# Kernel optimization log

Measured on AMD Instinct MI355X. Metric: run time of the kernel, lower is better.

The kernel has to match this reference:

```python
import jax, jax.numpy as jnp
import numpy as np

N, D, T, H, R = 1024, 6, 60, 64, 64
NEG = -10000.0
SLOPE = 0.01  # default LeakyReLU negative slope


def setup_inputs() -> dict:
    key = jax.random.key(0)
    ks = jax.random.split(key, 12)
    x = jax.random.normal(ks[0], (N, D * T), jnp.float32)
    relation_matrix = (jax.random.uniform(ks[1], (N, N, R)) < 0.02).astype(jnp.float32)
    s = 1.0 / np.sqrt(H)
    inp = {
        "x": x,
        "relation_matrix": relation_matrix,
        "W": jax.random.normal(ks[2], (2 * H + R, 1), jnp.float32) / np.sqrt(2 * H + R),
        "b": jnp.zeros((), jnp.float32),
        "fc_w": jax.random.normal(ks[3], (1, 2 * H), jnp.float32) * s,
        "fc_b": jnp.zeros((1,), jnp.float32),
        "Wih0": jax.random.normal(ks[4], (3 * H, D), jnp.float32) * s,
        "Whh0": jax.random.normal(ks[5], (3 * H, H), jnp.float32) * s,
        "bih0": jax.random.normal(ks[6], (3 * H,), jnp.float32) * s,
        "bhh0": jax.random.normal(ks[7], (3 * H,), jnp.float32) * s,
        "Wih1": jax.random.normal(ks[8], (3 * H, H), jnp.float32) * s,
        "Whh1": jax.random.normal(ks[9], (3 * H, H), jnp.float32) * s,
        "bih1": jax.random.normal(ks[10], (3 * H,), jnp.float32) * s,
        "bhh1": jax.random.normal(ks[11], (3 * H,), jnp.float32) * s,
    }
    return inp


def gru_layer(x, Wih, Whh, bih, bhh):
    # x: [N, T, in] -> outputs [N, T, H]; torch GRU gate order: r, z, n
    xg = x @ Wih.T + bih            # [N, T, 3H], input gates precomputed
    xg = jnp.swapaxes(xg, 0, 1)     # [T, N, 3H]

    def step(h, g):
        hg = h @ Whh.T + bhh
        xr, xz, xn = jnp.split(g, 3, axis=-1)
        hr, hz, hn = jnp.split(hg, 3, axis=-1)
        r = jax.nn.sigmoid(xr + hr)
        z = jax.nn.sigmoid(xz + hz)
        n = jnp.tanh(xn + r * hn)
        h = (1.0 - z) * n + z * h
        return h, h

    h0 = jnp.zeros((x.shape[0], Whh.shape[1]), x.dtype)
    _, ys = jax.lax.scan(step, h0, xg)
    return jnp.swapaxes(ys, 0, 1)   # [N, T, H]


def reference(x, relation_matrix, W, b, fc_w, fc_b,
              Wih0, Whh0, bih0, bhh0, Wih1, Whh1, bih1, bhh1):
    # [N, D*T] -> [N, T, D]
    xs = jnp.transpose(x.reshape(x.shape[0], D, -1), (0, 2, 1))
    h = gru_layer(xs, Wih0, Whh0, bih0, bhh0)
    h = gru_layer(h, Wih1, Whh1, bih1, bhh1)
    h = h[:, -1, :]                 # [N, H] last-step hidden

    # score[i,j] = cat(h_i, h_j, rel_ij) @ W + b, computed without the NxNx(2H+R) concat
    Wv = W[:, 0]
    sa = h @ Wv[:H]                              # [N]  (ei part)
    sb = h @ Wv[H:2 * H]                         # [N]  (hidden_batch part)
    sr = jnp.einsum('ijr,r->ij', relation_matrix, Wv[2 * H:])  # [N, N]
    weight = sa[:, None] + sb[None, :] + sr + b
    weight = jnp.where(weight >= 0, weight, SLOPE * weight)    # LeakyReLU

    mask = (relation_matrix.sum(-1) != 0).astype(h.dtype)      # [N, N]
    temp = mask * weight
    temp = jnp.where(temp == 0, NEG, temp)                     # faithful to torch ==0 fill
    valid = jax.nn.softmax(temp, axis=1) * mask

    agg = valid @ h                                            # [N, H]
    hidden = jnp.concatenate([h, agg], axis=1)                 # [N, 2H]
    pred_all = (hidden @ fc_w.T + fc_b).squeeze()
    return pred_all
```

## Files before the change

kernel.cpp:

```cpp
#include <hip/hip_runtime.h>
#include <cstddef>

#define NN 1024
#define DD 6
#define TT 60
#define HH 64
#define NEGV  (-10000.0f)
#define SLOPEV (0.01f)
#define GRUB 64
#define RELB 448
#define RELW (RELB * 8)
#define NGRP (NN * NN / 64)

#define BH0O  0
#define BH1O  1152
#define XH    2304
#define HEP   6144
#define SMEMF 7232

typedef _Float16 v8h __attribute__((ext_vector_type(8)));
typedef float    v4f __attribute__((ext_vector_type(4)));

#define MF(a, b, c) __builtin_amdgcn_mfma_f32_16x16x32_f16((a), (b), (c), 0, 0, 0)

__device__ __forceinline__ float sig_(float x)  { return 1.0f / (1.0f + __expf(-x)); }
__device__ __forceinline__ float tanh_(float x) { return 1.0f - 2.0f / (__expf(2.0f * x) + 1.0f); }
__device__ __forceinline__ float bcf_(const float a, const float b) {
    return __builtin_bit_cast(float, __builtin_amdgcn_cvt_pkrtz(a, b));
}
__device__ __forceinline__ v8h zero8() {
    v8h r;
    #pragma unroll
    for (int j = 0; j < 8; ++j) r[j] = (_Float16)0.f;
    return r;
}
__device__ __forceinline__ v8h pack8(const float* __restrict__ p) {
    v8h r;
    #pragma unroll
    for (int j = 0; j < 8; ++j) r[j] = (_Float16)p[j];
    return r;
}
__device__ __forceinline__ v8h pack6(const float* __restrict__ p) {
    v8h r = zero8();
    #pragma unroll
    for (int j = 0; j < 6; ++j) r[j] = (_Float16)p[j];
    return r;
}

__global__ __launch_bounds__(512)
void k_main(const float* __restrict__ x, const float* __restrict__ rel,
            const float* __restrict__ W, const float* __restrict__ fc_w,
            const float* __restrict__ Wih0, const float* __restrict__ Whh0,
            const float* __restrict__ bih0, const float* __restrict__ bhh0,
            const float* __restrict__ Wih1, const float* __restrict__ Whh1,
            const float* __restrict__ bih1, const float* __restrict__ bhh1,
            float* __restrict__ sa, float* __restrict__ sb,
            float* __restrict__ hdot, float* __restrict__ hb,
            float* __restrict__ sr, float* __restrict__ ssum)
{
    __shared__ float smem[SMEMF];
    const int tid = threadIdx.x;

    if (blockIdx.x >= GRUB) {
        const int lane = tid & 63;
        const int l16  = lane & 15;
        const int sub  = lane >> 4;
        const float4 wv4 = *(const float4*)(W + 2 * HH + l16 * 4);
        const unsigned wid = (unsigned)(blockIdx.x - GRUB) * 8 + (tid >> 6);
        for (unsigned g = wid; g < (unsigned)NGRP; g += RELW) {
            const float4* bp = (const float4*)(rel + (size_t)g * 4096) + lane;
            float4 v[16];
            #pragma unroll
            for (int q = 0; q < 16; ++q) v[q] = bp[q * 64];
            float dt[16], sm[16];
            #pragma unroll
            for (int q = 0; q < 16; ++q) {
                dt[q] = v[q].x * wv4.x + v[q].y * wv4.y + v[q].z * wv4.z + v[q].w * wv4.w;
                sm[q] = (v[q].x + v[q].y) + (v[q].z + v[q].w);
            }
            #pragma unroll
            for (int m = 1; m <= 8; m <<= 1) {
                #pragma unroll
                for (int q = 0; q < 16; ++q) {
                    dt[q] += __shfl_xor(dt[q], m);
                    sm[q] += __shfl_xor(sm[q], m);
                }
            }
            if (l16 == 0) {
                #pragma unroll
                for (int q = 0; q < 16; ++q) {
                    const unsigned p = g * 64 + q * 4 + sub;
                    sr[p]   = dt[q];
                    ssum[p] = sm[q];
                }
            }
        }
        return;
    }

    const int w    = tid >> 6;
    const int lane = tid & 63;
    const int quad = lane >> 4;
    const int mc   = lane & 15;
    const int nb   = blockIdx.x * 16;
    const bool isL0 = (w < 4);
    const int wt   = isL0 ? w : (w - 4);

    for (int idx = tid; idx < TT * 16; idx += 512) {
        const int t = idx >> 4, n = idx & 15;
        const float* xp = x + (size_t)(nb + n) * (DD * TT) + t;
        float4 pk;
        pk.x = bcf_(xp[0],   xp[60]);
        pk.y = bcf_(xp[120], xp[180]);
        pk.z = bcf_(xp[240], xp[300]);
        pk.w = 0.f;
        *(float4*)(smem + XH + idx * 4) = pk;
    }
    for (int idx = tid; idx < 2304; idx += 512) smem[idx] = 0.f;

    const int r0row = 16 * wt + mc;
    const int zrow  = 64 + 16 * wt + mc;
    const int nrow  = 128 + 16 * wt + mc;
    v8h F0 = zero8(), F1 = zero8(), F2 = zero8(), F3 = zero8();
    v8h F4 = zero8(), F5 = zero8(), F6 = zero8(), F7 = zero8();
    v8h F8 = zero8(), F9 = zero8(), F10 = zero8(), F11 = zero8();
    v8h Xr = zero8(), Xz = zero8(), Xn = zero8();
    if (isL0) {
        F0 = pack8(Whh0 + (size_t)r0row * HH + quad * 8);
        F1 = pack8(Whh0 + (size_t)r0row * HH + 32 + quad * 8);
        F2 = pack8(Whh0 + (size_t)zrow  * HH + quad * 8);
        F3 = pack8(Whh0 + (size_t)zrow  * HH + 32 + quad * 8);
        F4 = pack8(Whh0 + (size_t)nrow  * HH + quad * 8);
        F5 = pack8(Whh0 + (size_t)nrow  * HH + 32 + quad * 8);
        if (quad == 0) {
            Xr = pack6(Wih0 + r0row * DD);
            Xz = pack6(Wih0 + zrow  * DD);
            Xn = pack6(Wih0 + nrow  * DD);
        }
    } else {
        F0 = pack8(Wih1 + (size_t)r0row * HH + quad * 8);
        F1 = pack8(Wih1 + (size_t)r0row * HH + 32 + quad * 8);
        F2 = pack8(Whh1 + (size_t)r0row * HH + quad * 8);
        F3 = pack8(Whh1 + (size_t)r0row * HH + 32 + quad * 8);
        F4 = pack8(Wih1 + (size_t)zrow * HH + quad * 8);
        F5 = pack8(Wih1 + (size_t)zrow * HH + 32 + quad * 8);
        F6 = pack8(Whh1 + (size_t)zrow * HH + quad * 8);
        F7 = pack8(Whh1 + (size_t)zrow * HH + 32 + quad * 8);
        F8 = pack8(Wih1 + (size_t)nrow * HH + quad * 8);
        F9 = pack8(Wih1 + (size_t)nrow * HH + 32 + quad * 8);
        F10 = pack8(Whh1 + (size_t)nrow * HH + quad * 8);
        F11 = pack8(Whh1 + (size_t)nrow * HH + 32 + quad * 8);
    }

    float bR[4], bZ[4], bXn[4], bHn[4];
    #pragma unroll
    for (int e = 0; e < 4; ++e) {
        const int cr = 16 * wt + quad * 4 + e;
        if (isL0) {
            bR[e]  = bih0[cr] + bhh0[cr];
            bZ[e]  = bih0[64 + cr] + bhh0[64 + cr];
            bXn[e] = bih0[128 + cr];
            bHn[e] = bhh0[128 + cr];
        } else {
            bR[e]  = bih1[cr] + bhh1[cr];
            bZ[e]  = bih1[64 + cr] + bhh1[64 + cr];
            bXn[e] = bih1[128 + cr];
            bHn[e] = bhh1[128 + cr];
        }
    }

    float hp[4] = {0.f, 0.f, 0.f, 0.f};
    __syncthreads();

    auto ldb = [&](const float* basep, int win) -> v8h {
        return __builtin_bit_cast(v8h,
            *(const float4*)(basep + mc * 36 + win * 16 + quad * 4));
    };
    auto sth = [&](float* basep) {
        float2 pk;
        pk.x = bcf_(hp[0], hp[1]);
        pk.y = bcf_(hp[2], hp[3]);
        *(float2*)(basep + mc * 36 + 8 * wt + 2 * quad) = pk;
    };
    auto gupd = [&](const v4f& cr, const v4f& cz, const v4f& cx, const v4f& ch) {
        #pragma unroll
        for (int e = 0; e < 4; ++e) {
            const float r  = sig_(cr[e]);
            const float z  = sig_(cz[e]);
            const float nv = tanh_(cx[e] + r * ch[e]);
            hp[e] = (1.f - z) * nv + z * hp[e];
        }
    };

    for (int i = 0; i <= TT; ++i) {
        const int rbo = (i & 1) * 576;
        const int wbo = 576 - rbo;
        if (isL0) {
            if (i < TT) {
                const v8h b0 = ldb(smem + BH0O + rbo, 0);
                const v8h b1 = ldb(smem + BH0O + rbo, 1);
                const float4 xl = *(const float4*)(smem + XH + (i * 16 + mc) * 4);
                v8h bx = zero8();
                if (quad == 0) bx = __builtin_bit_cast(v8h, xl);

                v4f cr = {bR[0], bR[1], bR[2], bR[3]};
                cr = MF(F0, b0, cr); cr = MF(F1, b1, cr); cr = MF(Xr, bx, cr);
                v4f cz = {bZ[0], bZ[1], bZ[2], bZ[3]};
                cz = MF(F2, b0, cz); cz = MF(F3, b1, cz); cz = MF(Xz, bx, cz);
                v4f ch = {bHn[0], bHn[1], bHn[2], bHn[3]};
                ch = MF(F4, b0, ch); ch = MF(F5, b1, ch);
                v4f cx = {bXn[0], bXn[1], bXn[2], bXn[3]};
                cx = MF(Xn, bx, cx);

                gupd(cr, cz, cx, ch);
                sth(smem + BH0O + wbo);
            }
        } else {
            if (i >= 1) {
                const v8h g0 = ldb(smem + BH0O + rbo, 0);
                const v8h g1 = ldb(smem + BH0O + rbo, 1);
                const v8h g2 = ldb(smem + BH1O + rbo, 0);
                const v8h g3 = ldb(smem + BH1O + rbo, 1);

                v4f cr = {bR[0], bR[1], bR[2], bR[3]};
                cr = MF(F0, g0, cr); cr = MF(F1, g1, cr);
                cr = MF(F2, g2, cr); cr = MF(F3, g3, cr);
                v4f cz = {bZ[0], bZ[1], bZ[2], bZ[3]};
                cz = MF(F4, g0, cz); cz = MF(F5, g1, cz);
                cz = MF(F6, g2, cz); cz = MF(F7, g3, cz);
                v4f cx = {bXn[0], bXn[1], bXn[2], bXn[3]};
                cx = MF(F8, g0, cx); cx = MF(F9, g1, cx);
                v4f ch = {bHn[0], bHn[1], bHn[2], bHn[3]};
                ch = MF(F10, g2, ch); ch = MF(F11, g3, ch);

                gupd(cr, cz, cx, ch);
                sth(smem + BH1O + wbo);
            }
        }
        __syncthreads();
    }

    if (!isL0) {
        #pragma unroll
        for (int e = 0; e < 4; ++e)
            smem[HEP + (16 * wt + quad * 4 + e) * 17 + mc] = hp[e];
    }
    __syncthreads();
    if (isL0) {
        const int n = lane >> 2, p = lane & 3;
        const float* __restrict__ wp = (w == 0) ? W : (w == 1) ? (W + HH)
                                     : (w == 2) ? fc_w : (fc_w + HH);
        float v = 0.f;
        #pragma unroll
        for (int q = 0; q < 16; ++q) {
            const int j = p * 16 + q;
            v += smem[HEP + j * 17 + n] * wp[j];
        }
        v += __shfl_down(v, 2);
        v += __shfl_down(v, 1);
        if (p == 0) {
            float* dst = (w == 0) ? sa : (w == 1) ? sb : (w == 2) ? hdot : hb;
            dst[nb + n] = v;
        }
    }
}

__global__ __launch_bounds__(256)
void k2(const float* __restrict__ sa, const float* __restrict__ sb,
        const float* __restrict__ hdot, const float* __restrict__ hb,
        const float* __restrict__ sr, const float* __restrict__ ssum,
        const float* __restrict__ bscal, const float* __restrict__ fc_b,
        float* __restrict__ out)
{
    __shared__ float red[12];
    const int i   = blockIdx.x;
    const int tid = threadIdx.x;
    const int j4  = tid * 4;
    const float sai = sa[i] + bscal[0];

    const float4 srv = *(const float4*)(sr   + (size_t)i * NN + j4);
    const float4 ssv = *(const float4*)(ssum + (size_t)i * NN + j4);
    const float4 sbv = *(const float4*)(sb + j4);

    float tv[4], mk[4];
    float mloc = -3.4e38f;
    {
        const float srq[4] = {srv.x, srv.y, srv.z, srv.w};
        const float ssq[4] = {ssv.x, ssv.y, ssv.z, ssv.w};
        const float sbq[4] = {sbv.x, sbv.y, sbv.z, sbv.w};
        #pragma unroll
        for (int q = 0; q < 4; ++q) {
            float wv = sai + sbq[q] + srq[q];
            wv = (wv >= 0.0f) ? wv : SLOPEV * wv;
            const float m = (ssq[q] != 0.0f) ? 1.0f : 0.0f;
            float tt = m * wv;
            tt = (tt == 0.0f) ? NEGV : tt;
            tv[q] = tt; mk[q] = m;
            mloc = fmaxf(mloc, tt);
        }
    }
    #pragma unroll
    for (int off = 32; off >= 1; off >>= 1) mloc = fmaxf(mloc, __shfl_xor(mloc, off));
    if ((tid & 63) == 0) red[tid >> 6] = mloc;
    __syncthreads();
    const float mx = fmaxf(fmaxf(red[0], red[1]), fmaxf(red[2], red[3]));

    const float4 hbv = *(const float4*)(hb + j4);
    const float hbq[4] = {hbv.x, hbv.y, hbv.z, hbv.w};
    float sloc = 0.0f, vloc = 0.0f;
    #pragma unroll
    for (int q = 0; q < 4; ++q) {
        const float e = __expf(tv[q] - mx);
        sloc += e;
        vloc += e * mk[q] * hbq[q];
    }
    #pragma unroll
    for (int off = 32; off >= 1; off >>= 1) {
        sloc += __shfl_xor(sloc, off);
        vloc += __shfl_xor(vloc, off);
    }
    if ((tid & 63) == 0) { red[4 + (tid >> 6)] = sloc; red[8 + (tid >> 6)] = vloc; }
    __syncthreads();
    if (tid == 0) {
        const float denom = red[4] + red[5] + red[6] + red[7];
        const float vsum  = red[8] + red[9] + red[10] + red[11];
        out[i] = hdot[i] + vsum / denom + fc_b[0];
    }
}

extern "C" void kernel_launch(void* const* d_in, const int* in_sizes, int n_in,
                              void* d_out, int out_size, void* d_ws, size_t ws_size,
                              hipStream_t stream)
{
    const float* x     = (const float*)d_in[0];
    const float* rel   = (const float*)d_in[1];
    const float* W     = (const float*)d_in[2];
    const float* b     = (const float*)d_in[3];
    const float* fc_w  = (const float*)d_in[4];
    const float* fc_b  = (const float*)d_in[5];
    const float* Wih0  = (const float*)d_in[6];
    const float* Whh0  = (const float*)d_in[7];
    const float* bih0  = (const float*)d_in[8];
    const float* bhh0  = (const float*)d_in[9];
    const float* Wih1  = (const float*)d_in[10];
    const float* Whh1  = (const float*)d_in[11];
    const float* bih1  = (const float*)d_in[12];
    const float* bhh1  = (const float*)d_in[13];

    float* ws   = (float*)d_ws;
    float* sa   = ws;
    float* sb   = sa   + NN;
    float* hdot = sb   + NN;
    float* hb   = hdot + NN;
    float* sr   = hb   + NN;
    float* ssum = sr   + (size_t)NN * NN;

    k_main<<<GRUB + RELB, 512, 0, stream>>>(x, rel, W, fc_w,
                                            Wih0, Whh0, bih0, bhh0,
                                            Wih1, Whh1, bih1, bhh1,
                                            sa, sb, hdot, hb, sr, ssum);
    k2<<<NN, 256, 0, stream>>>(sa, sb, hdot, hb, sr, ssum,
                               b, fc_b, (float*)d_out);
}
```

Baseline: 384.7 us.

## Move relation-tensor reduction into softmax kernel, drop global sr/ssum intermediates

Removes the relation-reduction blocks from the GRU kernel and instead computes each row's relation dot-product and mask sum inside the softmax kernel, keeping them in shared memory. This eliminates writing and re-reading two NxN float intermediates in global memory. In exchange, the large relation-tensor read no longer overlaps the latency-bound GRU recurrence and now runs after it.

```diff
diff --git a/kernel.cpp b/kernel.cpp
--- a/kernel.cpp
+++ b/kernel.cpp
@@ -8,9 +8,6 @@
 #define NEGV  (-10000.0f)
 #define SLOPEV (0.01f)
 #define GRUB 64
-#define RELB 448
-#define RELW (RELB * 8)
-#define NGRP (NN * NN / 64)
 
 #define BH0O  0
 #define BH1O  1152
@@ -48,55 +45,17 @@
 }
 
 __global__ __launch_bounds__(512)
-void k_main(const float* __restrict__ x, const float* __restrict__ rel,
-            const float* __restrict__ W, const float* __restrict__ fc_w,
-            const float* __restrict__ Wih0, const float* __restrict__ Whh0,
-            const float* __restrict__ bih0, const float* __restrict__ bhh0,
-            const float* __restrict__ Wih1, const float* __restrict__ Whh1,
-            const float* __restrict__ bih1, const float* __restrict__ bhh1,
-            float* __restrict__ sa, float* __restrict__ sb,
-            float* __restrict__ hdot, float* __restrict__ hb,
-            float* __restrict__ sr, float* __restrict__ ssum)
+void k_gru(const float* __restrict__ x,
+           const float* __restrict__ W, const float* __restrict__ fc_w,
+           const float* __restrict__ Wih0, const float* __restrict__ Whh0,
+           const float* __restrict__ bih0, const float* __restrict__ bhh0,
+           const float* __restrict__ Wih1, const float* __restrict__ Whh1,
+           const float* __restrict__ bih1, const float* __restrict__ bhh1,
+           float* __restrict__ sa, float* __restrict__ sb,
+           float* __restrict__ hdot, float* __restrict__ hb)
 {
     __shared__ float smem[SMEMF];
     const int tid = threadIdx.x;
-
-    if (blockIdx.x >= GRUB) {
-        const int lane = tid & 63;
-        const int l16  = lane & 15;
-        const int sub  = lane >> 4;
-        const float4 wv4 = *(const float4*)(W + 2 * HH + l16 * 4);
-        const unsigned wid = (unsigned)(blockIdx.x - GRUB) * 8 + (tid >> 6);
-        for (unsigned g = wid; g < (unsigned)NGRP; g += RELW) {
-            const float4* bp = (const float4*)(rel + (size_t)g * 4096) + lane;
-            float4 v[16];
-            #pragma unroll
-            for (int q = 0; q < 16; ++q) v[q] = bp[q * 64];
-            float dt[16], sm[16];
-            #pragma unroll
-            for (int q = 0; q < 16; ++q) {
-                dt[q] = v[q].x * wv4.x + v[q].y * wv4.y + v[q].z * wv4.z + v[q].w * wv4.w;
-                sm[q] = (v[q].x + v[q].y) + (v[q].z + v[q].w);
-            }
-            #pragma unroll
-            for (int m = 1; m <= 8; m <<= 1) {
-                #pragma unroll
-                for (int q = 0; q < 16; ++q) {
-                    dt[q] += __shfl_xor(dt[q], m);
-                    sm[q] += __shfl_xor(sm[q], m);
-                }
-            }
-            if (l16 == 0) {
-                #pragma unroll
-                for (int q = 0; q < 16; ++q) {
-                    const unsigned p = g * 64 + q * 4 + sub;
-                    sr[p]   = dt[q];
-                    ssum[p] = sm[q];
-                }
-            }
-        }
-        return;
-    }
 
     const int w    = tid >> 6;
     const int lane = tid & 63;
@@ -266,20 +225,66 @@
 }
 
 __global__ __launch_bounds__(256)
-void k2(const float* __restrict__ sa, const float* __restrict__ sb,
-        const float* __restrict__ hdot, const float* __restrict__ hb,
-        const float* __restrict__ sr, const float* __restrict__ ssum,
-        const float* __restrict__ bscal, const float* __restrict__ fc_b,
-        float* __restrict__ out)
+void k2f(const float* __restrict__ rel, const float* __restrict__ W,
+         const float* __restrict__ sa, const float* __restrict__ sb,
+         const float* __restrict__ hdot, const float* __restrict__ hb,
+         const float* __restrict__ bscal, const float* __restrict__ fc_b,
+         float* __restrict__ out)
 {
+    __shared__ float srL[NN];
+    __shared__ float smL[NN];
     __shared__ float red[12];
-    const int i   = blockIdx.x;
-    const int tid = threadIdx.x;
-    const int j4  = tid * 4;
+
+    const int i    = blockIdx.x;
+    const int tid  = threadIdx.x;
+    const int wv   = tid >> 6;
+    const int lane = tid & 63;
+    const int l16  = lane & 15;
+    const int sub  = lane >> 4;
+
+    const float4 wv4 = *(const float4*)(W + 2 * HH + l16 * 4);
+    #pragma unroll
+    for (int gi = 0; gi < 4; ++gi) {
+        const int g = wv * 4 + gi;
+        const float4* bp = (const float4*)(rel + (size_t)i * NN * 64
+                                               + (size_t)g * 4096) + lane;
+        float dt[16], sm[16];
+        #pragma unroll
+        for (int c = 0; c < 2; ++c) {
+            float4 v[8];
+            #pragma unroll
+            for (int q = 0; q < 8; ++q) v[q] = bp[(c * 8 + q) * 64];
+            #pragma unroll
+            for (int q = 0; q < 8; ++q) {
+                dt[c * 8 + q] = v[q].x * wv4.x + v[q].y * wv4.y
+                              + v[q].z * wv4.z + v[q].w * wv4.w;
+                sm[c * 8 + q] = (v[q].x + v[q].y) + (v[q].z + v[q].w);
+            }
+        }
+        #pragma unroll
+        for (int m = 1; m <= 8; m <<= 1) {
+            #pragma unroll
+            for (int q = 0; q < 16; ++q) {
+                dt[q] += __shfl_xor(dt[q], m);
+                sm[q] += __shfl_xor(sm[q], m);
+            }
+        }
+        if (l16 == 0) {
+            #pragma unroll
+            for (int q = 0; q < 16; ++q) {
+                const int p = g * 64 + q * 4 + sub;
+                srL[p] = dt[q];
+                smL[p] = sm[q];
+            }
+        }
+    }
+    __syncthreads();
+
+    const int j4 = tid * 4;
     const float sai = sa[i] + bscal[0];
 
-    const float4 srv = *(const float4*)(sr   + (size_t)i * NN + j4);
-    const float4 ssv = *(const float4*)(ssum + (size_t)i * NN + j4);
+    const float4 srv = *(const float4*)(srL + j4);
+    const float4 ssv = *(const float4*)(smL + j4);
     const float4 sbv = *(const float4*)(sb + j4);
 
     float tv[4], mk[4];
@@ -290,10 +295,10 @@
         const float sbq[4] = {sbv.x, sbv.y, sbv.z, sbv.w};
         #pragma unroll
         for (int q = 0; q < 4; ++q) {
-            float wv = sai + sbq[q] + srq[q];
-            wv = (wv >= 0.0f) ? wv : SLOPEV * wv;
+            float wq = sai + sbq[q] + srq[q];
+            wq = (wq >= 0.0f) ? wq : SLOPEV * wq;
             const float m = (ssq[q] != 0.0f) ? 1.0f : 0.0f;
-            float tt = m * wv;
+            float tt = m * wq;
             tt = (tt == 0.0f) ? NEGV : tt;
             tv[q] = tt; mk[q] = m;
             mloc = fmaxf(mloc, tt);
@@ -352,13 +357,11 @@
     float* sb   = sa   + NN;
     float* hdot = sb   + NN;
     float* hb   = hdot + NN;
-    float* sr   = hb   + NN;
-    float* ssum = sr   + (size_t)NN * NN;
-
-    k_main<<<GRUB + RELB, 512, 0, stream>>>(x, rel, W, fc_w,
-                                            Wih0, Whh0, bih0, bhh0,
-                                            Wih1, Whh1, bih1, bhh1,
-                                            sa, sb, hdot, hb, sr, ssum);
-    k2<<<NN, 256, 0, stream>>>(sa, sb, hdot, hb, sr, ssum,
-                               b, fc_b, (float*)d_out);
-}
+
+    k_gru<<<GRUB, 512, 0, stream>>>(x, W, fc_w,
+                                    Wih0, Whh0, bih0, bhh0,
+                                    Wih1, Whh1, bih1, bhh1,
+                                    sa, sb, hdot, hb);
+    k2f<<<NN, 256, 0, stream>>>(rel, W, sa, sb, hdot, hb,
+                                b, fc_b, (float*)d_out);
+}
```

Measured after the change: 453.1 us. +17.8%, slower.
